# Kernel tuning notes

Hardware: AMD Instinct MI355X
Metric: run time of the kernel (lower is better)

Reference implementation:

```python
import jax, jax.numpy as jnp
import numpy as np

N = 50000
E = 800000
IN_DIM, HID, OUT = 128, 256, 256


def setup_inputs() -> dict:
    key = jax.random.key(0)
    ks = jax.random.split(key, 6)
    x = jax.random.normal(ks[0], (N, IN_DIM), dtype=jnp.float32)
    edge_index = jax.random.randint(ks[1], (2, E), 0, N, dtype=jnp.int64)
    W1 = jax.random.normal(ks[2], (IN_DIM, HID), dtype=jnp.float32) / np.sqrt(IN_DIM)
    b1 = jnp.zeros((HID,), dtype=jnp.float32)
    W2 = jax.random.normal(ks[3], (HID, OUT), dtype=jnp.float32) / np.sqrt(HID)
    b2 = jnp.zeros((OUT,), dtype=jnp.float32)
    return {"x": x, "edge_index": edge_index, "W1": W1, "b1": b1, "W2": W2, "b2": b2}


def _gcn_conv(x, edge_index, W, b):
    """PyG GCNConv: add self-loops, symmetric deg^-1/2 norm, linear, scatter-add, bias."""
    n = x.shape[0]
    loops = jnp.arange(n, dtype=edge_index.dtype)
    src = jnp.concatenate([edge_index[0], loops])  # [E+N]
    dst = jnp.concatenate([edge_index[1], loops])  # [E+N]
    deg = jax.ops.segment_sum(jnp.ones(src.shape[0], dtype=x.dtype), dst, num_segments=n)
    dinv = jnp.where(deg > 0, jax.lax.rsqrt(deg), jnp.zeros_like(deg))
    norm = dinv[src] * dinv[dst]  # [E+N]
    h = x @ W  # [N, out] small GEMM before gather (PyG order)
    msg = h[src] * norm[:, None]  # [E+N, out] -- dominant memory traffic
    out = jax.ops.segment_sum(msg, dst, num_segments=n)
    return out + b


def reference(x, edge_index, W1, b1, W2, b2):
    h = jax.nn.relu(_gcn_conv(x, edge_index, W1, b1))
    # dropout is identity in eval mode
    out = _gcn_conv(h, edge_index, W2, b2)
    # F.normalize(p=2, dim=-1, eps=1e-12)
    nrm = jnp.maximum(jnp.linalg.norm(out, axis=-1, keepdims=True), 1e-12)
    return out / nrm
```

## Files before the change

kernel.cpp:

```cpp
#include <hip/hip_runtime.h>
#include <hip/hip_bf16.h>


#define NNODE 50000
#define FDIM 256
#define SCAN_CHUNK 2048

typedef __attribute__((ext_vector_type(8))) short short8;
typedef __attribute__((ext_vector_type(4))) float f32x4;

__device__ __forceinline__ float bf2f(unsigned short u) {
    union { unsigned int i; float f; } c;
    c.i = ((unsigned int)u) << 16;
    return c.f;
}
__device__ __forceinline__ unsigned short f2bf(float f) {
    __hip_bfloat16 h = __float2bfloat16(f);
    return *reinterpret_cast<unsigned short*>(&h);
}

__global__ void count_kernel(const int* __restrict__ ei, int* __restrict__ counts, int E) {
    int e = blockIdx.x * blockDim.x + threadIdx.x;
    if (e < E) atomicAdd(&counts[ei[E + e]], 1);
}

__global__ __launch_bounds__(256) void scan_part1(const int* __restrict__ counts,
                                                  int* __restrict__ bsum, int n) {
    __shared__ int ws[4];
    int b = blockIdx.x, t = threadIdx.x;
    int base = b * SCAN_CHUNK + t * 8;
    int s = 0;
#pragma unroll
    for (int j = 0; j < 8; ++j) {
        int i = base + j;
        if (i < n) s += counts[i];
    }
#pragma unroll
    for (int off = 32; off >= 1; off >>= 1) s += __shfl_xor(s, off, 64);
    if ((t & 63) == 0) ws[t >> 6] = s;
    __syncthreads();
    if (t == 0) bsum[b] = ws[0] + ws[1] + ws[2] + ws[3];
}

__global__ void scan_part2(const int* __restrict__ bsum, int* __restrict__ boff,
                           int* __restrict__ row_ptr, int nb, int n) {
    int l = threadIdx.x;
    int v = (l < nb) ? bsum[l] : 0;
    int incl = v;
#pragma unroll
    for (int off = 1; off < 64; off <<= 1) {
        int u = __shfl_up(incl, off, 64);
        if (l >= off) incl += u;
    }
    if (l < nb) boff[l] = incl - v;
    if (l == nb - 1) row_ptr[n] = incl;
}

__global__ __launch_bounds__(256) void scan_part3(const int* __restrict__ counts,
                                                  const int* __restrict__ boff,
                                                  int* __restrict__ row_ptr,
                                                  int* __restrict__ cursor, int n) {
    __shared__ int ws[4];
    int b = blockIdx.x, t = threadIdx.x, lane = t & 63, wid = t >> 6;
    int base = b * SCAN_CHUNK + t * 8;
    int v[8];
    int s = 0;
#pragma unroll
    for (int j = 0; j < 8; ++j) {
        int i = base + j;
        v[j] = (i < n) ? counts[i] : 0;
        s += v[j];
    }
    int incl = s;
#pragma unroll
    for (int off = 1; off < 64; off <<= 1) {
        int u = __shfl_up(incl, off, 64);
        if (lane >= off) incl += u;
    }
    if (lane == 63) ws[wid] = incl;
    __syncthreads();
    int woff = 0;
    for (int u = 0; u < wid; ++u) woff += ws[u];
    int ex = boff[b] + woff + incl - s;
#pragma unroll
    for (int j = 0; j < 8; ++j) {
        int i = base + j;
        if (i < n) { row_ptr[i] = ex; cursor[i] = ex; }
        ex += v[j];
    }
}

__global__ void dinv_kernel(const int* __restrict__ counts, float* __restrict__ dinv, int n) {
    int i = blockIdx.x * blockDim.x + threadIdx.x;
    if (i < n) dinv[i] = rsqrtf((float)(counts[i] + 1));
}

__global__ void fill_kernel(const int* __restrict__ ei, const float* __restrict__ dinv,
                            int* __restrict__ cursor, int2* __restrict__ edata, int E) {
    int e = blockIdx.x * blockDim.x + threadIdx.x;
    if (e < E) {
        int s = ei[e];
        int d = ei[E + e];
        int pos = atomicAdd(&cursor[d], 1);
        float nm = dinv[s] * dinv[d];
        edata[pos] = make_int2(s, __float_as_int(nm));
    }
}

template <int K>
__global__ void wconv_kernel(const float* __restrict__ W, unsigned short* __restrict__ Wf) {
    int idx = blockIdx.x * blockDim.x + threadIdx.x;
    if (idx >= (K / 8) * 256) return;
    int g = idx >> 8, c = idx & 255;
    ushort4 lo = make_ushort4(f2bf(W[(8 * g + 0) * 256 + c]), f2bf(W[(8 * g + 1) * 256 + c]),
                              f2bf(W[(8 * g + 2) * 256 + c]), f2bf(W[(8 * g + 3) * 256 + c]));
    ushort4 hi = make_ushort4(f2bf(W[(8 * g + 4) * 256 + c]), f2bf(W[(8 * g + 5) * 256 + c]),
                              f2bf(W[(8 * g + 6) * 256 + c]), f2bf(W[(8 * g + 7) * 256 + c]));
    *reinterpret_cast<ushort4*>(&Wf[(size_t)idx * 8]) = lo;
    *reinterpret_cast<ushort4*>(&Wf[(size_t)idx * 8 + 4]) = hi;
}

template <int K, typename T>
__global__ __launch_bounds__(256) void gemm_mfma(const T* __restrict__ X,
                                                 const unsigned short* __restrict__ Wf,
                                                 unsigned short* __restrict__ H, int n) {
    __shared__ unsigned short As[128 * K];
    __shared__ unsigned short Bs[(K / 8) * 128 * 8];
    int t = threadIdx.x;
    int row0 = blockIdx.x * 128;
    int cb = blockIdx.y;

    if constexpr (sizeof(T) == 4) {
#pragma unroll
        for (int i = 0; i < (128 * K) / (4 * 256); ++i) {
            int o = 4 * (t + 256 * i);
            int row = o / K, k = o % K;
            int srow = row0 + row;
            float4 v = make_float4(0.f, 0.f, 0.f, 0.f);
            if (srow < n) v = *reinterpret_cast<const float4*>(&X[(size_t)srow * K + k]);
            ushort4 p = make_ushort4(f2bf(v.x), f2bf(v.y), f2bf(v.z), f2bf(v.w));
            int gx = (k >> 3) ^ (row & 7);
            *reinterpret_cast<ushort4*>(&As[row * K + gx * 8 + (k & 7)]) = p;
        }
    } else {
#pragma unroll
        for (int i = 0; i < (128 * K) / (8 * 256); ++i) {
            int o = 8 * (t + 256 * i);
            int row = o / K, k = o % K;
            int srow = row0 + row;
            uint4 v = make_uint4(0u, 0u, 0u, 0u);
            if (srow < n) v = *reinterpret_cast<const uint4*>(&X[(size_t)srow * K + k]);
            int gx = (k >> 3) ^ (row & 7);
            *reinterpret_cast<uint4*>(&As[row * K + gx * 8]) = v;
        }
    }
#pragma unroll
    for (int i = 0; i < ((K / 8) * 128) / 256; ++i) {
        int idx = t + 256 * i;
        int g = idx >> 7, c = idx & 127;
        *reinterpret_cast<uint4*>(&Bs[idx * 8]) =
            *reinterpret_cast<const uint4*>(&Wf[((size_t)g * 256 + cb * 128 + c) * 8]);
    }
    __syncthreads();

    int lane = t & 63, wv = t >> 6;
    int rw = wv >> 1, cw = wv & 1;
    int l15 = lane & 15, lhi = lane >> 4;
    f32x4 zero = {0.f, 0.f, 0.f, 0.f};
    f32x4 acc[4][4];
#pragma unroll
    for (int rf = 0; rf < 4; ++rf)
#pragma unroll
        for (int cf = 0; cf < 4; ++cf) acc[rf][cf] = zero;

#pragma unroll
    for (int s = 0; s < K / 32; ++s) {
        int g = 4 * s + lhi;
        short8 a[4], b[4];
#pragma unroll
        for (int rf = 0; rf < 4; ++rf) {
            int row = 64 * rw + 16 * rf + l15;
            a[rf] = *reinterpret_cast<const short8*>(&As[row * K + (g ^ (row & 7)) * 8]);
        }
#pragma unroll
        for (int cf = 0; cf < 4; ++cf) {
            int c = 64 * cw + 16 * cf + l15;
            b[cf] = *reinterpret_cast<const short8*>(&Bs[(g * 128 + c) * 8]);
        }
#pragma unroll
        for (int rf = 0; rf < 4; ++rf)
#pragma unroll
            for (int cf = 0; cf < 4; ++cf)
                acc[rf][cf] = __builtin_amdgcn_mfma_f32_16x16x32_bf16(a[rf], b[cf], acc[rf][cf], 0, 0, 0);
    }

#pragma unroll
    for (int rf = 0; rf < 4; ++rf)
#pragma unroll
        for (int cf = 0; cf < 4; ++cf) {
            f32x4 a = acc[rf][cf];
            int col = cb * 128 + 64 * cw + 16 * cf + l15;
#pragma unroll
            for (int j = 0; j < 4; ++j) {
                int row = row0 + 64 * rw + 16 * rf + 4 * lhi + j;
                if (row < n) H[(size_t)row * 256 + col] = f2bf(a[j]);
            }
        }
}

__device__ __forceinline__ void agg_core(const unsigned short* __restrict__ hb,
                                         const int* __restrict__ rowp,
                                         const int2* __restrict__ edata,
                                         const float* __restrict__ dinv,
                                         const float* __restrict__ bias,
                                         int node, int lane,
                                         float& a0, float& a1, float& a2, float& a3) {
    float di = dinv[node];
    float d2 = di * di;
    ushort4 sv = *(reinterpret_cast<const ushort4*>(hb + (size_t)node * FDIM) + lane);
    float4 bv = *(reinterpret_cast<const float4*>(bias) + lane);
    a0 = fmaf(bf2f(sv.x), d2, bv.x);
    a1 = fmaf(bf2f(sv.y), d2, bv.y);
    a2 = fmaf(bf2f(sv.z), d2, bv.z);
    a3 = fmaf(bf2f(sv.w), d2, bv.w);
    int beg = rowp[node], end = rowp[node + 1];
#pragma unroll 4
    for (int e = beg; e < end; ++e) {
        int2 ed = edata[e];
        float nm = __int_as_float(ed.y);
        ushort4 v = *(reinterpret_cast<const ushort4*>(hb + (size_t)ed.x * FDIM) + lane);
        a0 = fmaf(bf2f(v.x), nm, a0);
        a1 = fmaf(bf2f(v.y), nm, a1);
        a2 = fmaf(bf2f(v.z), nm, a2);
        a3 = fmaf(bf2f(v.w), nm, a3);
    }
}

__global__ __launch_bounds__(256) void agg_relu_kernel(const unsigned short* __restrict__ hb,
                                                       const int* __restrict__ rowp,
                                                       const int2* __restrict__ edata,
                                                       const float* __restrict__ dinv,
                                                       const float* __restrict__ bias,
                                                       unsigned short* __restrict__ outB, int n) {
    int node = (blockIdx.x * blockDim.x + threadIdx.x) >> 6;
    int lane = threadIdx.x & 63;
    if (node >= n) return;
    float a0, a1, a2, a3;
    agg_core(hb, rowp, edata, dinv, bias, node, lane, a0, a1, a2, a3);
    ushort4 o = make_ushort4(f2bf(fmaxf(a0, 0.f)), f2bf(fmaxf(a1, 0.f)),
                             f2bf(fmaxf(a2, 0.f)), f2bf(fmaxf(a3, 0.f)));
    *(reinterpret_cast<ushort4*>(outB + (size_t)node * FDIM) + lane) = o;
}

__global__ __launch_bounds__(256) void agg_norm_kernel(const unsigned short* __restrict__ hb,
                                                       const int* __restrict__ rowp,
                                                       const int2* __restrict__ edata,
                                                       const float* __restrict__ dinv,
                                                       const float* __restrict__ bias,
                                                       float* __restrict__ out, int n) {
    int node = (blockIdx.x * blockDim.x + threadIdx.x) >> 6;
    int lane = threadIdx.x & 63;
    if (node >= n) return;
    float a0, a1, a2, a3;
    agg_core(hb, rowp, edata, dinv, bias, node, lane, a0, a1, a2, a3);
    float ss = a0 * a0 + a1 * a1 + a2 * a2 + a3 * a3;
#pragma unroll
    for (int off = 32; off >= 1; off >>= 1) ss += __shfl_xor(ss, off, 64);
    float rinv = 1.f / fmaxf(sqrtf(ss), 1e-12f);
    f32x4 o = {a0 * rinv, a1 * rinv, a2 * rinv, a3 * rinv};
    __builtin_nontemporal_store(o, reinterpret_cast<f32x4*>(out + (size_t)node * FDIM) + lane);
}

extern "C" void kernel_launch(void* const* d_in, const int* in_sizes, int n_in,
                              void* d_out, int out_size, void* d_ws, size_t ws_size,
                              hipStream_t stream) {
    const float* x  = (const float*)d_in[0];
    const int*   ei = (const int*)d_in[1];
    const float* W1 = (const float*)d_in[2];
    const float* b1 = (const float*)d_in[3];
    const float* W2 = (const float*)d_in[4];
    const float* b2 = (const float*)d_in[5];
    float* out = (float*)d_out;

    const int N = NNODE;
    const int E = in_sizes[1] / 2;
    const int NB = (N + SCAN_CHUNK - 1) / SCAN_CHUNK;

    char* ws = (char*)d_ws;
    size_t off = 0;
    auto alloc = [&](size_t bytes) -> void* {
        void* p = ws + off;
        off = (off + bytes + 255) & ~(size_t)255;
        return p;
    };
    unsigned short* Hbf = (unsigned short*)alloc((size_t)N * FDIM * 2);
    unsigned short* Bbf = (unsigned short*)alloc((size_t)N * FDIM * 2);
    unsigned short* Wf1 = (unsigned short*)alloc((size_t)(128 / 8) * 256 * 8 * 2);
    unsigned short* Wf2 = (unsigned short*)alloc((size_t)(256 / 8) * 256 * 8 * 2);
    int*   counts = (int*)alloc((size_t)N * 4);
    int*   rowp   = (int*)alloc((size_t)(N + 1) * 4);
    int*   cursor = (int*)alloc((size_t)N * 4);
    float* dinv   = (float*)alloc((size_t)N * 4);
    int2*  edata  = (int2*)alloc((size_t)E * 8);
    int*   bsum   = (int*)alloc((size_t)NB * 4);
    int*   boff   = (int*)alloc((size_t)NB * 4);

    wconv_kernel<128><<<(16 * 256 + 255) / 256, 256, 0, stream>>>(W1, Wf1);
    wconv_kernel<256><<<(32 * 256 + 255) / 256, 256, 0, stream>>>(W2, Wf2);

    hipMemsetAsync(counts, 0, (size_t)N * 4, stream);
    count_kernel<<<(E + 255) / 256, 256, 0, stream>>>(ei, counts, E);
    scan_part1<<<NB, 256, 0, stream>>>(counts, bsum, N);
    scan_part2<<<1, 64, 0, stream>>>(bsum, boff, rowp, NB, N);
    scan_part3<<<NB, 256, 0, stream>>>(counts, boff, rowp, cursor, N);
    dinv_kernel<<<(N + 255) / 256, 256, 0, stream>>>(counts, dinv, N);
    fill_kernel<<<(E + 255) / 256, 256, 0, stream>>>(ei, dinv, cursor, edata, E);

    dim3 ggrid((N + 127) / 128, 2);
    gemm_mfma<128, float><<<ggrid, 256, 0, stream>>>(x, Wf1, Hbf, N);
    agg_relu_kernel<<<(N * 64 + 255) / 256, 256, 0, stream>>>(Hbf, rowp, edata, dinv, b1, Bbf, N);
    gemm_mfma<256, unsigned short><<<ggrid, 256, 0, stream>>>(Bbf, Wf2, Hbf, N);
    agg_norm_kernel<<<(N * 64 + 255) / 256, 256, 0, stream>>>(Hbf, rowp, edata, dinv, b2, out, N);
}
```

Measured before the change: 279.5 us.

## Split edges across half-waves in aggregation, retile GEMM, fuse small setup kernels

Aggregation now has each half-wave take a different edge and load 16-byte rows, then combines the two halves with a cross-lane shuffle. This doubles the gathers in flight per wave and widens each load. The GEMM switches to 64-row blocks that cover all 256 columns and read weight fragments straight from global memory instead of staging them in LDS, so the input tile is loaded only once. The dinv computation is folded into scan_part3 and the two weight-conversion launches are merged into one, removing two launches. The cost is that odd-degree nodes leave a half-wave idle on its last step, and the B-operand reads in the GEMM now depend on cache hits.

```diff
diff --git a/kernel.cpp b/kernel.cpp
--- a/kernel.cpp
+++ b/kernel.cpp
@@ -12,6 +12,16 @@
 __device__ __forceinline__ float bf2f(unsigned short u) {
     union { unsigned int i; float f; } c;
     c.i = ((unsigned int)u) << 16;
+    return c.f;
+}
+__device__ __forceinline__ float bflo(unsigned int u) {
+    union { unsigned int i; float f; } c;
+    c.i = u << 16;
+    return c.f;
+}
+__device__ __forceinline__ float bfhi(unsigned int u) {
+    union { unsigned int i; float f; } c;
+    c.i = u & 0xFFFF0000u;
     return c.f;
 }
 __device__ __forceinline__ unsigned short f2bf(float f) {
@@ -59,7 +69,8 @@
 __global__ __launch_bounds__(256) void scan_part3(const int* __restrict__ counts,
                                                   const int* __restrict__ boff,
                                                   int* __restrict__ row_ptr,
-                                                  int* __restrict__ cursor, int n) {
+                                                  int* __restrict__ cursor,
+                                                  float* __restrict__ dinv, int n) {
     __shared__ int ws[4];
     int b = blockIdx.x, t = threadIdx.x, lane = t & 63, wid = t >> 6;
     int base = b * SCAN_CHUNK + t * 8;
@@ -85,14 +96,13 @@
 #pragma unroll
     for (int j = 0; j < 8; ++j) {
         int i = base + j;
-        if (i < n) { row_ptr[i] = ex; cursor[i] = ex; }
+        if (i < n) {
+            row_ptr[i] = ex;
+            cursor[i] = ex;
+            dinv[i] = rsqrtf((float)(v[j] + 1));
+        }
         ex += v[j];
     }
-}
-
-__global__ void dinv_kernel(const int* __restrict__ counts, float* __restrict__ dinv, int n) {
-    int i = blockIdx.x * blockDim.x + threadIdx.x;
-    if (i < n) dinv[i] = rsqrtf((float)(counts[i] + 1));
 }
 
 __global__ void fill_kernel(const int* __restrict__ ei, const float* __restrict__ dinv,
@@ -107,10 +117,19 @@
     }
 }
 
-template <int K>
-__global__ void wconv_kernel(const float* __restrict__ W, unsigned short* __restrict__ Wf) {
+__global__ void wconv_kernel(const float* __restrict__ W1, unsigned short* __restrict__ Wf1,
+                             const float* __restrict__ W2, unsigned short* __restrict__ Wf2) {
     int idx = blockIdx.x * blockDim.x + threadIdx.x;
-    if (idx >= (K / 8) * 256) return;
+    const float* W;
+    unsigned short* Wf;
+    if (idx < 16 * 256) {
+        W = W1; Wf = Wf1;
+    } else if (idx < (16 + 32) * 256) {
+        idx -= 16 * 256;
+        W = W2; Wf = Wf2;
+    } else {
+        return;
+    }
     int g = idx >> 8, c = idx & 255;
     ushort4 lo = make_ushort4(f2bf(W[(8 * g + 0) * 256 + c]), f2bf(W[(8 * g + 1) * 256 + c]),
                               f2bf(W[(8 * g + 2) * 256 + c]), f2bf(W[(8 * g + 3) * 256 + c]));
@@ -124,15 +143,13 @@
 __global__ __launch_bounds__(256) void gemm_mfma(const T* __restrict__ X,
                                                  const unsigned short* __restrict__ Wf,
                                                  unsigned short* __restrict__ H, int n) {
-    __shared__ unsigned short As[128 * K];
-    __shared__ unsigned short Bs[(K / 8) * 128 * 8];
+    __shared__ unsigned short As[64 * K];
     int t = threadIdx.x;
-    int row0 = blockIdx.x * 128;
-    int cb = blockIdx.y;
+    int row0 = blockIdx.x * 64;
 
     if constexpr (sizeof(T) == 4) {
 #pragma unroll
-        for (int i = 0; i < (128 * K) / (4 * 256); ++i) {
+        for (int i = 0; i < (64 * K) / (4 * 256); ++i) {
             int o = 4 * (t + 256 * i);
             int row = o / K, k = o % K;
             int srow = row0 + row;
@@ -144,7 +161,7 @@
         }
     } else {
 #pragma unroll
-        for (int i = 0; i < (128 * K) / (8 * 256); ++i) {
+        for (int i = 0; i < (64 * K) / (8 * 256); ++i) {
             int o = 8 * (t + 256 * i);
             int row = o / K, k = o % K;
             int srow = row0 + row;
@@ -154,17 +171,9 @@
             *reinterpret_cast<uint4*>(&As[row * K + gx * 8]) = v;
         }
     }
-#pragma unroll
-    for (int i = 0; i < ((K / 8) * 128) / 256; ++i) {
-        int idx = t + 256 * i;
-        int g = idx >> 7, c = idx & 127;
-        *reinterpret_cast<uint4*>(&Bs[idx * 8]) =
-            *reinterpret_cast<const uint4*>(&Wf[((size_t)g * 256 + cb * 128 + c) * 8]);
-    }
     __syncthreads();
 
     int lane = t & 63, wv = t >> 6;
-    int rw = wv >> 1, cw = wv & 1;
     int l15 = lane & 15, lhi = lane >> 4;
     f32x4 zero = {0.f, 0.f, 0.f, 0.f};
     f32x4 acc[4][4];
@@ -179,13 +188,13 @@
         short8 a[4], b[4];
 #pragma unroll
         for (int rf = 0; rf < 4; ++rf) {
-            int row = 64 * rw + 16 * rf + l15;
+            int row = 16 * rf + l15;
             a[rf] = *reinterpret_cast<const short8*>(&As[row * K + (g ^ (row & 7)) * 8]);
         }
 #pragma unroll
         for (int cf = 0; cf < 4; ++cf) {
-            int c = 64 * cw + 16 * cf + l15;
-            b[cf] = *reinterpret_cast<const short8*>(&Bs[(g * 128 + c) * 8]);
+            int c = 64 * wv + 16 * cf + l15;
+            b[cf] = *reinterpret_cast<const short8*>(&Wf[((size_t)g * 256 + c) * 8]);
         }
 #pragma unroll
         for (int rf = 0; rf < 4; ++rf)
@@ -199,10 +208,10 @@
 #pragma unroll
         for (int cf = 0; cf < 4; ++cf) {
             f32x4 a = acc[rf][cf];
-            int col = cb * 128 + 64 * cw + 16 * cf + l15;
+            int col = 64 * wv + 16 * cf + l15;
 #pragma unroll
             for (int j = 0; j < 4; ++j) {
-                int row = row0 + 64 * rw + 16 * rf + 4 * lhi + j;
+                int row = row0 + 16 * rf + 4 * lhi + j;
                 if (row < n) H[(size_t)row * 256 + col] = f2bf(a[j]);
             }
         }
@@ -213,27 +222,43 @@
                                          const int2* __restrict__ edata,
                                          const float* __restrict__ dinv,
                                          const float* __restrict__ bias,
-                                         int node, int lane,
-                                         float& a0, float& a1, float& a2, float& a3) {
+                                         int node, int lane, float acc[8]) {
+    int half = lane >> 5;
+    int l31 = lane & 31;
     float di = dinv[node];
-    float d2 = di * di;
-    ushort4 sv = *(reinterpret_cast<const ushort4*>(hb + (size_t)node * FDIM) + lane);
-    float4 bv = *(reinterpret_cast<const float4*>(bias) + lane);
-    a0 = fmaf(bf2f(sv.x), d2, bv.x);
-    a1 = fmaf(bf2f(sv.y), d2, bv.y);
-    a2 = fmaf(bf2f(sv.z), d2, bv.z);
-    a3 = fmaf(bf2f(sv.w), d2, bv.w);
+    float scale = half ? 0.f : 1.f;
+    float d2 = di * di * scale;
+    uint4 sv = *(reinterpret_cast<const uint4*>(hb + (size_t)node * FDIM) + l31);
+    float4 bv0 = *(reinterpret_cast<const float4*>(bias) + 2 * l31);
+    float4 bv1 = *(reinterpret_cast<const float4*>(bias) + 2 * l31 + 1);
+    acc[0] = fmaf(bflo(sv.x), d2, bv0.x * scale);
+    acc[1] = fmaf(bfhi(sv.x), d2, bv0.y * scale);
+    acc[2] = fmaf(bflo(sv.y), d2, bv0.z * scale);
+    acc[3] = fmaf(bfhi(sv.y), d2, bv0.w * scale);
+    acc[4] = fmaf(bflo(sv.z), d2, bv1.x * scale);
+    acc[5] = fmaf(bfhi(sv.z), d2, bv1.y * scale);
+    acc[6] = fmaf(bflo(sv.w), d2, bv1.z * scale);
+    acc[7] = fmaf(bfhi(sv.w), d2, bv1.w * scale);
     int beg = rowp[node], end = rowp[node + 1];
-#pragma unroll 4
-    for (int e = beg; e < end; ++e) {
-        int2 ed = edata[e];
-        float nm = __int_as_float(ed.y);
-        ushort4 v = *(reinterpret_cast<const ushort4*>(hb + (size_t)ed.x * FDIM) + lane);
-        a0 = fmaf(bf2f(v.x), nm, a0);
-        a1 = fmaf(bf2f(v.y), nm, a1);
-        a2 = fmaf(bf2f(v.z), nm, a2);
-        a3 = fmaf(bf2f(v.w), nm, a3);
-    }
+#pragma unroll 2
+    for (int e = beg; e < end; e += 2) {
+        int ee = e + half;
+        bool valid = ee < end;
+        int2 ed = edata[valid ? ee : e];
+        float nm = valid ? __int_as_float(ed.y) : 0.f;
+        int src = valid ? ed.x : node;
+        uint4 v = *(reinterpret_cast<const uint4*>(hb + (size_t)src * FDIM) + l31);
+        acc[0] = fmaf(bflo(v.x), nm, acc[0]);
+        acc[1] = fmaf(bfhi(v.x), nm, acc[1]);
+        acc[2] = fmaf(bflo(v.y), nm, acc[2]);
+        acc[3] = fmaf(bfhi(v.y), nm, acc[3]);
+        acc[4] = fmaf(bflo(v.z), nm, acc[4]);
+        acc[5] = fmaf(bfhi(v.z), nm, acc[5]);
+        acc[6] = fmaf(bflo(v.w), nm, acc[6]);
+        acc[7] = fmaf(bfhi(v.w), nm, acc[7]);
+    }
+#pragma unroll
+    for (int j = 0; j < 8; ++j) acc[j] += __shfl_xor(acc[j], 32, 64);
 }
 
 __global__ __launch_bounds__(256) void agg_relu_kernel(const unsigned short* __restrict__ hb,
@@ -245,11 +270,13 @@
     int node = (blockIdx.x * blockDim.x + threadIdx.x) >> 6;
     int lane = threadIdx.x & 63;
     if (node >= n) return;
-    float a0, a1, a2, a3;
-    agg_core(hb, rowp, edata, dinv, bias, node, lane, a0, a1, a2, a3);
-    ushort4 o = make_ushort4(f2bf(fmaxf(a0, 0.f)), f2bf(fmaxf(a1, 0.f)),
-                             f2bf(fmaxf(a2, 0.f)), f2bf(fmaxf(a3, 0.f)));
-    *(reinterpret_cast<ushort4*>(outB + (size_t)node * FDIM) + lane) = o;
+    float acc[8];
+    agg_core(hb, rowp, edata, dinv, bias, node, lane, acc);
+    int half = lane >> 5, l31 = lane & 63 & 31;
+    int j0 = 4 * half;
+    ushort4 o = make_ushort4(f2bf(fmaxf(acc[j0 + 0], 0.f)), f2bf(fmaxf(acc[j0 + 1], 0.f)),
+                             f2bf(fmaxf(acc[j0 + 2], 0.f)), f2bf(fmaxf(acc[j0 + 3], 0.f)));
+    *reinterpret_cast<ushort4*>(outB + (size_t)node * FDIM + l31 * 8 + j0) = o;
 }
 
 __global__ __launch_bounds__(256) void agg_norm_kernel(const unsigned short* __restrict__ hb,
@@ -261,14 +288,18 @@
     int node = (blockIdx.x * blockDim.x + threadIdx.x) >> 6;
     int lane = threadIdx.x & 63;
     if (node >= n) return;
-    float a0, a1, a2, a3;
-    agg_core(hb, rowp, edata, dinv, bias, node, lane, a0, a1, a2, a3);
-    float ss = a0 * a0 + a1 * a1 + a2 * a2 + a3 * a3;
-#pragma unroll
-    for (int off = 32; off >= 1; off >>= 1) ss += __shfl_xor(ss, off, 64);
+    float acc[8];
+    agg_core(hb, rowp, edata, dinv, bias, node, lane, acc);
+    float ss = 0.f;
+#pragma unroll
+    for (int j = 0; j < 8; ++j) ss = fmaf(acc[j], acc[j], ss);
+#pragma unroll
+    for (int off = 16; off >= 1; off >>= 1) ss += __shfl_xor(ss, off, 64);
     float rinv = 1.f / fmaxf(sqrtf(ss), 1e-12f);
-    f32x4 o = {a0 * rinv, a1 * rinv, a2 * rinv, a3 * rinv};
-    __builtin_nontemporal_store(o, reinterpret_cast<f32x4*>(out + (size_t)node * FDIM) + lane);
+    int half = lane >> 5, l31 = lane & 31;
+    int j0 = 4 * half;
+    f32x4 o = {acc[j0 + 0] * rinv, acc[j0 + 1] * rinv, acc[j0 + 2] * rinv, acc[j0 + 3] * rinv};
+    __builtin_nontemporal_store(o, reinterpret_cast<f32x4*>(out + (size_t)node * FDIM + l31 * 8 + j0));
 }
 
 extern "C" void kernel_launch(void* const* d_in, const int* in_sizes, int n_in,
@@ -305,20 +336,17 @@
     int*   bsum   = (int*)alloc((size_t)NB * 4);
     int*   boff   = (int*)alloc((size_t)NB * 4);
 
-    wconv_kernel<128><<<(16 * 256 + 255) / 256, 256, 0, stream>>>(W1, Wf1);
-    wconv_kernel<256><<<(32 * 256 + 255) / 256, 256, 0, stream>>>(W2, Wf2);
+    wconv_kernel<<<(48 * 256 + 255) / 256, 256, 0, stream>>>(W1, Wf1, W2, Wf2);
 
     hipMemsetAsync(counts, 0, (size_t)N * 4, stream);
     count_kernel<<<(E + 255) / 256, 256, 0, stream>>>(ei, counts, E);
     scan_part1<<<NB, 256, 0, stream>>>(counts, bsum, N);
     scan_part2<<<1, 64, 0, stream>>>(bsum, boff, rowp, NB, N);
-    scan_part3<<<NB, 256, 0, stream>>>(counts, boff, rowp, cursor, N);
-    dinv_kernel<<<(N + 255) / 256, 256, 0, stream>>>(counts, dinv, N);
+    scan_part3<<<NB, 256, 0, stream>>>(counts, boff, rowp, cursor, dinv, N);
     fill_kernel<<<(E + 255) / 256, 256, 0, stream>>>(ei, dinv, cursor, edata, E);
 
-    dim3 ggrid((N + 127) / 128, 2);
-    gemm_mfma<128, float><<<ggrid, 256, 0, stream>>>(x, Wf1, Hbf, N);
+    gemm_mfma<128, float><<<(N + 63) / 64, 256, 0, stream>>>(x, Wf1, Hbf, N);
     agg_relu_kernel<<<(N * 64 + 255) / 256, 256, 0, stream>>>(Hbf, rowp, edata, dinv, b1, Bbf, N);
-    gemm_mfma<256, unsigned short><<<ggrid, 256, 0, stream>>>(Bbf, Wf2, Hbf, N);
+    gemm_mfma<256, unsigned short><<<(N + 63) / 64, 256, 0, stream>>>(Bbf, Wf2, Hbf, N);
     agg_norm_kernel<<<(N * 64 + 255) / 256, 256, 0, stream>>>(Hbf, rowp, edata, dinv, b2, out, N);
 }
```

Measured after the change: 253.1 us. -9.5%, faster.

## Fuse setup kernels, widen GEMM to full columns, split layer-1 aggregation by feature half

Applied to the files above, without the earlier changes.

Folds the dinv computation into scan_part3 and merges the two weight-conversion launches into one, cutting launch count. The GEMM now uses 512-thread blocks that cover all 256 output columns, so the activation tile is loaded once, and B fragments are read straight from global memory instead of being staged in LDS. The layer-1 aggregation is split into two feature halves per node, each wave processing two edges at a time, to raise parallelism and keep the gathered rows cache-local. The risks are uncached global B reads inside the MFMA loop and extra shuffle and branch overhead in the aggregation.

```diff
diff --git a/kernel.cpp b/kernel.cpp
--- a/kernel.cpp
+++ b/kernel.cpp
@@ -59,7 +59,8 @@
 __global__ __launch_bounds__(256) void scan_part3(const int* __restrict__ counts,
                                                   const int* __restrict__ boff,
                                                   int* __restrict__ row_ptr,
-                                                  int* __restrict__ cursor, int n) {
+                                                  int* __restrict__ cursor,
+                                                  float* __restrict__ dinv, int n) {
     __shared__ int ws[4];
     int b = blockIdx.x, t = threadIdx.x, lane = t & 63, wid = t >> 6;
     int base = b * SCAN_CHUNK + t * 8;
@@ -85,14 +86,13 @@
 #pragma unroll
     for (int j = 0; j < 8; ++j) {
         int i = base + j;
-        if (i < n) { row_ptr[i] = ex; cursor[i] = ex; }
+        if (i < n) {
+            row_ptr[i] = ex;
+            cursor[i] = ex;
+            dinv[i] = rsqrtf((float)(v[j] + 1));
+        }
         ex += v[j];
     }
-}
-
-__global__ void dinv_kernel(const int* __restrict__ counts, float* __restrict__ dinv, int n) {
-    int i = blockIdx.x * blockDim.x + threadIdx.x;
-    if (i < n) dinv[i] = rsqrtf((float)(counts[i] + 1));
 }
 
 __global__ void fill_kernel(const int* __restrict__ ei, const float* __restrict__ dinv,
@@ -107,10 +107,19 @@
     }
 }
 
-template <int K>
-__global__ void wconv_kernel(const float* __restrict__ W, unsigned short* __restrict__ Wf) {
+__global__ void wconv_kernel(const float* __restrict__ W1, unsigned short* __restrict__ Wf1,
+                             const float* __restrict__ W2, unsigned short* __restrict__ Wf2) {
     int idx = blockIdx.x * blockDim.x + threadIdx.x;
-    if (idx >= (K / 8) * 256) return;
+    const float* W;
+    unsigned short* Wf;
+    if (idx < 16 * 256) {
+        W = W1; Wf = Wf1;
+    } else if (idx < (16 + 32) * 256) {
+        idx -= 16 * 256;
+        W = W2; Wf = Wf2;
+    } else {
+        return;
+    }
     int g = idx >> 8, c = idx & 255;
     ushort4 lo = make_ushort4(f2bf(W[(8 * g + 0) * 256 + c]), f2bf(W[(8 * g + 1) * 256 + c]),
                               f2bf(W[(8 * g + 2) * 256 + c]), f2bf(W[(8 * g + 3) * 256 + c]));
@@ -121,19 +130,17 @@
 }
 
 template <int K, typename T>
-__global__ __launch_bounds__(256) void gemm_mfma(const T* __restrict__ X,
-                                                 const unsigned short* __restrict__ Wf,
-                                                 unsigned short* __restrict__ H, int n) {
+__global__ __launch_bounds__(512, 4) void gemm_mfma(const T* __restrict__ X,
+                                                    const unsigned short* __restrict__ Wf,
+                                                    unsigned short* __restrict__ H, int n) {
     __shared__ unsigned short As[128 * K];
-    __shared__ unsigned short Bs[(K / 8) * 128 * 8];
     int t = threadIdx.x;
     int row0 = blockIdx.x * 128;
-    int cb = blockIdx.y;
 
     if constexpr (sizeof(T) == 4) {
 #pragma unroll
-        for (int i = 0; i < (128 * K) / (4 * 256); ++i) {
-            int o = 4 * (t + 256 * i);
+        for (int i = 0; i < (128 * K) / (4 * 512); ++i) {
+            int o = 4 * (t + 512 * i);
             int row = o / K, k = o % K;
             int srow = row0 + row;
             float4 v = make_float4(0.f, 0.f, 0.f, 0.f);
@@ -144,8 +151,8 @@
         }
     } else {
 #pragma unroll
-        for (int i = 0; i < (128 * K) / (8 * 256); ++i) {
-            int o = 8 * (t + 256 * i);
+        for (int i = 0; i < (128 * K) / (8 * 512); ++i) {
+            int o = 8 * (t + 512 * i);
             int row = o / K, k = o % K;
             int srow = row0 + row;
             uint4 v = make_uint4(0u, 0u, 0u, 0u);
@@ -154,17 +161,10 @@
             *reinterpret_cast<uint4*>(&As[row * K + gx * 8]) = v;
         }
     }
-#pragma unroll
-    for (int i = 0; i < ((K / 8) * 128) / 256; ++i) {
-        int idx = t + 256 * i;
-        int g = idx >> 7, c = idx & 127;
-        *reinterpret_cast<uint4*>(&Bs[idx * 8]) =
-            *reinterpret_cast<const uint4*>(&Wf[((size_t)g * 256 + cb * 128 + c) * 8]);
-    }
     __syncthreads();
 
     int lane = t & 63, wv = t >> 6;
-    int rw = wv >> 1, cw = wv & 1;
+    int rw = wv >> 2, cw = wv & 3;
     int l15 = lane & 15, lhi = lane >> 4;
     f32x4 zero = {0.f, 0.f, 0.f, 0.f};
     f32x4 acc[4][4];
@@ -185,7 +185,7 @@
 #pragma unroll
         for (int cf = 0; cf < 4; ++cf) {
             int c = 64 * cw + 16 * cf + l15;
-            b[cf] = *reinterpret_cast<const short8*>(&Bs[(g * 128 + c) * 8]);
+            b[cf] = *reinterpret_cast<const short8*>(&Wf[((size_t)g * 256 + c) * 8]);
         }
 #pragma unroll
         for (int rf = 0; rf < 4; ++rf)
@@ -199,7 +199,7 @@
 #pragma unroll
         for (int cf = 0; cf < 4; ++cf) {
             f32x4 a = acc[rf][cf];
-            int col = cb * 128 + 64 * cw + 16 * cf + l15;
+            int col = 64 * cw + 16 * cf + l15;
 #pragma unroll
             for (int j = 0; j < 4; ++j) {
                 int row = row0 + 64 * rw + 16 * rf + 4 * lhi + j;
@@ -208,21 +208,71 @@
         }
 }
 
-__device__ __forceinline__ void agg_core(const unsigned short* __restrict__ hb,
-                                         const int* __restrict__ rowp,
-                                         const int2* __restrict__ edata,
-                                         const float* __restrict__ dinv,
-                                         const float* __restrict__ bias,
-                                         int node, int lane,
-                                         float& a0, float& a1, float& a2, float& a3) {
+__global__ __launch_bounds__(256) void agg_relu_split(const unsigned short* __restrict__ hb,
+                                                      const int* __restrict__ rowp,
+                                                      const int2* __restrict__ edata,
+                                                      const float* __restrict__ dinv,
+                                                      const float* __restrict__ bias,
+                                                      unsigned short* __restrict__ outB, int n) {
+    int b = blockIdx.x;
+    int fhalf = (b >> 2) & 1;
+    int chunk = ((b >> 3) << 2) | (b & 3);
+    int node = chunk * 4 + (threadIdx.x >> 6);
+    if (node >= n) return;
+    int lane = threadIdx.x & 63;
+    int half = lane >> 5, l31 = lane & 31;
+    int fb = fhalf * 128 + l31 * 4;
+    float di = dinv[node];
+    float scale = half ? 0.f : 1.f;
+    float d2 = di * di * scale;
+    ushort4 sv = *reinterpret_cast<const ushort4*>(hb + (size_t)node * FDIM + fb);
+    float4 bv = *reinterpret_cast<const float4*>(bias + fb);
+    float a0 = fmaf(bf2f(sv.x), d2, bv.x * scale);
+    float a1 = fmaf(bf2f(sv.y), d2, bv.y * scale);
+    float a2 = fmaf(bf2f(sv.z), d2, bv.z * scale);
+    float a3 = fmaf(bf2f(sv.w), d2, bv.w * scale);
+    int beg = rowp[node], end = rowp[node + 1];
+#pragma unroll 2
+    for (int e = beg; e < end; e += 2) {
+        int ee = e + half;
+        bool valid = ee < end;
+        int2 ed = edata[valid ? ee : e];
+        float nm = valid ? __int_as_float(ed.y) : 0.f;
+        int src = valid ? ed.x : node;
+        ushort4 v = *reinterpret_cast<const ushort4*>(hb + (size_t)src * FDIM + fb);
+        a0 = fmaf(bf2f(v.x), nm, a0);
+        a1 = fmaf(bf2f(v.y), nm, a1);
+        a2 = fmaf(bf2f(v.z), nm, a2);
+        a3 = fmaf(bf2f(v.w), nm, a3);
+    }
+    a0 += __shfl_xor(a0, 32, 64);
+    a1 += __shfl_xor(a1, 32, 64);
+    a2 += __shfl_xor(a2, 32, 64);
+    a3 += __shfl_xor(a3, 32, 64);
+    if (half == 0) {
+        ushort4 o = make_ushort4(f2bf(fmaxf(a0, 0.f)), f2bf(fmaxf(a1, 0.f)),
+                                 f2bf(fmaxf(a2, 0.f)), f2bf(fmaxf(a3, 0.f)));
+        *reinterpret_cast<ushort4*>(outB + (size_t)node * FDIM + fb) = o;
+    }
+}
+
+__global__ __launch_bounds__(256) void agg_norm_kernel(const unsigned short* __restrict__ hb,
+                                                       const int* __restrict__ rowp,
+                                                       const int2* __restrict__ edata,
+                                                       const float* __restrict__ dinv,
+                                                       const float* __restrict__ bias,
+                                                       float* __restrict__ out, int n) {
+    int node = (blockIdx.x * blockDim.x + threadIdx.x) >> 6;
+    int lane = threadIdx.x & 63;
+    if (node >= n) return;
     float di = dinv[node];
     float d2 = di * di;
     ushort4 sv = *(reinterpret_cast<const ushort4*>(hb + (size_t)node * FDIM) + lane);
     float4 bv = *(reinterpret_cast<const float4*>(bias) + lane);
-    a0 = fmaf(bf2f(sv.x), d2, bv.x);
-    a1 = fmaf(bf2f(sv.y), d2, bv.y);
-    a2 = fmaf(bf2f(sv.z), d2, bv.z);
-    a3 = fmaf(bf2f(sv.w), d2, bv.w);
+    float a0 = fmaf(bf2f(sv.x), d2, bv.x);
+    float a1 = fmaf(bf2f(sv.y), d2, bv.y);
+    float a2 = fmaf(bf2f(sv.z), d2, bv.z);
+    float a3 = fmaf(bf2f(sv.w), d2, bv.w);
     int beg = rowp[node], end = rowp[node + 1];
 #pragma unroll 4
     for (int e = beg; e < end; ++e) {
@@ -234,35 +284,6 @@
         a2 = fmaf(bf2f(v.z), nm, a2);
         a3 = fmaf(bf2f(v.w), nm, a3);
     }
-}
-
-__global__ __launch_bounds__(256) void agg_relu_kernel(const unsigned short* __restrict__ hb,
-                                                       const int* __restrict__ rowp,
-                                                       const int2* __restrict__ edata,
-                                                       const float* __restrict__ dinv,
-                                                       const float* __restrict__ bias,
-                                                       unsigned short* __restrict__ outB, int n) {
-    int node = (blockIdx.x * blockDim.x + threadIdx.x) >> 6;
-    int lane = threadIdx.x & 63;
-    if (node >= n) return;
-    float a0, a1, a2, a3;
-    agg_core(hb, rowp, edata, dinv, bias, node, lane, a0, a1, a2, a3);
-    ushort4 o = make_ushort4(f2bf(fmaxf(a0, 0.f)), f2bf(fmaxf(a1, 0.f)),
-                             f2bf(fmaxf(a2, 0.f)), f2bf(fmaxf(a3, 0.f)));
-    *(reinterpret_cast<ushort4*>(outB + (size_t)node * FDIM) + lane) = o;
-}
-
-__global__ __launch_bounds__(256) void agg_norm_kernel(const unsigned short* __restrict__ hb,
-                                                       const int* __restrict__ rowp,
-                                                       const int2* __restrict__ edata,
-                                                       const float* __restrict__ dinv,
-                                                       const float* __restrict__ bias,
-                                                       float* __restrict__ out, int n) {
-    int node = (blockIdx.x * blockDim.x + threadIdx.x) >> 6;
-    int lane = threadIdx.x & 63;
-    if (node >= n) return;
-    float a0, a1, a2, a3;
-    agg_core(hb, rowp, edata, dinv, bias, node, lane, a0, a1, a2, a3);
     float ss = a0 * a0 + a1 * a1 + a2 * a2 + a3 * a3;
 #pragma unroll
     for (int off = 32; off >= 1; off >>= 1) ss += __shfl_xor(ss, off, 64);
@@ -305,20 +326,18 @@
     int*   bsum   = (int*)alloc((size_t)NB * 4);
     int*   boff   = (int*)alloc((size_t)NB * 4);
 
-    wconv_kernel<128><<<(16 * 256 + 255) / 256, 256, 0, stream>>>(W1, Wf1);
-    wconv_kernel<256><<<(32 * 256 + 255) / 256, 256, 0, stream>>>(W2, Wf2);
+    wconv_kernel<<<(48 * 256 + 255) / 256, 256, 0, stream>>>(W1, Wf1, W2, Wf2);
 
     hipMemsetAsync(counts, 0, (size_t)N * 4, stream);
     count_kernel<<<(E + 255) / 256, 256, 0, stream>>>(ei, counts, E);
     scan_part1<<<NB, 256, 0, stream>>>(counts, bsum, N);
     scan_part2<<<1, 64, 0, stream>>>(bsum, boff, rowp, NB, N);
-    scan_part3<<<NB, 256, 0, stream>>>(counts, boff, rowp, cursor, N);
-    dinv_kernel<<<(N + 255) / 256, 256, 0, stream>>>(counts, dinv, N);
+    scan_part3<<<NB, 256, 0, stream>>>(counts, boff, rowp, cursor, dinv, N);
     fill_kernel<<<(E + 255) / 256, 256, 0, stream>>>(ei, dinv, cursor, edata, E);
 
-    dim3 ggrid((N + 127) / 128, 2);
-    gemm_mfma<128, float><<<ggrid, 256, 0, stream>>>(x, Wf1, Hbf, N);
-    agg_relu_kernel<<<(N * 64 + 255) / 256, 256, 0, stream>>>(Hbf, rowp, edata, dinv, b1, Bbf, N);
-    gemm_mfma<256, unsigned short><<<ggrid, 256, 0, stream>>>(Bbf, Wf2, Hbf, N);
+    gemm_mfma<128, float><<<(N + 127) / 128, 512, 0, stream>>>(x, Wf1, Hbf, N);
+    int chunks = (N + 3) / 4;
+    agg_relu_split<<<2 * chunks, 256, 0, stream>>>(Hbf, rowp, edata, dinv, b1, Bbf, N);
+    gemm_mfma<256, unsigned short><<<(N + 127) / 128, 512, 0, stream>>>(Bbf, Wf2, Hbf, N);
     agg_norm_kernel<<<(N * 64 + 255) / 256, 256, 0, stream>>>(Hbf, rowp, edata, dinv, b2, out, N);
 }
```

Result: faster. 271.7 us (-2.8%).
